# Kernel optimization log

Measured on AMD Instinct MI355X. Metric: run time of the kernel, lower is better.

## Reference

```python
import jax, jax.numpy as jnp
import numpy as np

D_MODEL = 512
H = 8


def setup_inputs() -> dict:
    key = jax.random.key(0)
    ks = jax.random.split(key, 11)
    B, L, D = 8, 1024, D_MODEL
    s = 1.0 / np.sqrt(D)
    return {
        "q": jax.random.normal(ks[0], (B, L, D), jnp.float32),
        "k": jax.random.normal(ks[1], (B, L, D), jnp.float32),
        "v": jax.random.normal(ks[2], (B, L, D), jnp.float32),
        "Wq": jax.random.normal(ks[3], (D, D), jnp.float32) * s,
        "bq": jnp.zeros((D,), jnp.float32),
        "Wk": jax.random.normal(ks[4], (D, D), jnp.float32) * s,
        "bk": jnp.zeros((D,), jnp.float32),
        "Wv": jax.random.normal(ks[5], (D, D), jnp.float32) * s,
        "bv": jnp.zeros((D,), jnp.float32),
        "Wo": jax.random.normal(ks[6], (D, D), jnp.float32) * s,
        "bo": jnp.zeros((D,), jnp.float32),
    }


def _split_heads(x, h):
    B, L, D = x.shape
    return x.reshape(B, L, h, D // h).transpose(0, 2, 1, 3)  # (B,h,L,dk)


def reference(q, k, v, Wq, bq, Wk, bk, Wv, bv, Wo, bo):
    B, L, D = q.shape
    dk = D // H
    qw = q @ Wq + bq
    kw = k @ Wk + bk
    vw = q @ Wv + bv  # faithful to source bug: dense_v applied to q, not v
    qh = _split_heads(qw, H)
    kh = _split_heads(kw, H)
    vh = _split_heads(vw, H)
    scale = jnp.asarray(1.0 / np.sqrt(dk), qh.dtype)
    scores = jnp.einsum("bhqd,bhkd->bhqk", qh, kh) * scale  # (B,h,L,L)
    attn = jax.nn.softmax(scores, axis=-1)
    ctx = jnp.einsum("bhqk,bhkd->bhqd", attn, vh)  # (B,h,L,dk)
    out = ctx.transpose(0, 2, 1, 3).reshape(B, L, D) @ Wo + bo
    return out, attn
```

## Files before the change

### kernel.cpp

```cpp
#include <hip/hip_runtime.h>

typedef unsigned short u16;
typedef __bf16 bf16x8 __attribute__((ext_vector_type(8)));
typedef unsigned short u16x8 __attribute__((ext_vector_type(8)));
typedef unsigned short u16x4 __attribute__((ext_vector_type(4)));
typedef float f32x4 __attribute__((ext_vector_type(4)));

#define MFMA16(a, b, c) __builtin_amdgcn_mfma_f32_16x16x32_bf16(a, b, c, 0, 0, 0)

__device__ __forceinline__ u16 f2bf(float f) {
    union { float f; unsigned u; } v; v.f = f;
    unsigned r = v.u + 0x7fffu + ((v.u >> 16) & 1u);
    return (u16)(r >> 16);
}
__device__ __forceinline__ float bf2f(u16 u) {
    union { unsigned u; float f; } v; v.u = (unsigned)u << 16;
    return v.f;
}

__global__ __launch_bounds__(256) void wtrans(const float* Wq, const float* Wk,
                                              const float* Wv, const float* Wo, u16* WT) {
    __shared__ float t[32][33];
    const int z = blockIdx.z;
    const float* W = (z == 0) ? Wq : (z == 1) ? Wk : (z == 2) ? Wv : Wo;
    u16* out = WT + (size_t)z * 512 * 512;
    const int tx = threadIdx.x, ty = threadIdx.y;
    const int k0 = blockIdx.y * 32, n0 = blockIdx.x * 32;
#pragma unroll
    for (int p = 0; p < 4; ++p)
        t[ty + 8 * p][tx] = W[(size_t)(k0 + ty + 8 * p) * 512 + n0 + tx];
    __syncthreads();
#pragma unroll
    for (int p = 0; p < 4; ++p) {
        const int n = n0 + ty + 8 * p;
        out[(size_t)n * 512 + k0 + tx] = f2bf(t[tx][ty + 8 * p]);
    }
}

__global__ __launch_bounds__(256) void qkconv(const float* q, const float* k, u16* qb, u16* kb) {
    const size_t n4 = (size_t)8192 * 512 / 4;
    const size_t stride = (size_t)gridDim.x * 256;
    for (size_t i = (size_t)blockIdx.x * 256 + threadIdx.x; i < 2 * n4; i += stride) {
        const float4 v = (i < n4) ? ((const float4*)q)[i] : ((const float4*)k)[i - n4];
        u16x4 o;
        o[0] = f2bf(v.x); o[1] = f2bf(v.y); o[2] = f2bf(v.z); o[3] = f2bf(v.w);
        if (i < n4) ((u16x4*)qb)[i] = o; else ((u16x4*)kb)[i - n4] = o;
    }
}

template <bool C_F32>
__device__ __forceinline__ void gemm_core(const u16* A, const u16* Bt,
                                          const float* bias, void* Cp,
                                          int bm, int bn) {
    __shared__ u16 As[128 * 72];
    __shared__ u16 Bs[128 * 72];
    const int tid  = threadIdx.x;
    const int lane = tid & 63;
    const int w    = tid >> 6;
    const int wm   = (w >> 1) * 64;
    const int wn   = (w & 1) * 64;
    const int col  = lane & 15;
    const int quad = lane >> 4;

    f32x4 acc[4][4] = {};

    for (int kt = 0; kt < 512; kt += 64) {
        __syncthreads();
        {
            const int kg = (tid & 7) * 8;
            const int r0 = tid >> 3;
#pragma unroll
            for (int p = 0; p < 4; ++p) {
                const int r = r0 + p * 32;
                *(u16x8*)(As + r * 72 + kg) =
                    *(const u16x8*)(A + (size_t)(bm * 128 + r) * 512 + kt + kg);
                *(u16x8*)(Bs + r * 72 + kg) =
                    *(const u16x8*)(Bt + (size_t)(bn * 128 + r) * 512 + kt + kg);
            }
        }
        __syncthreads();
#pragma unroll
        for (int ks = 0; ks < 2; ++ks) {
            const int k0 = ks * 32 + quad * 8;
            bf16x8 af[4], bfr[4];
#pragma unroll
            for (int i = 0; i < 4; ++i)
                af[i] = __builtin_bit_cast(bf16x8, *(const u16x8*)(As + (wm + i * 16 + col) * 72 + k0));
#pragma unroll
            for (int j = 0; j < 4; ++j)
                bfr[j] = __builtin_bit_cast(bf16x8, *(const u16x8*)(Bs + (wn + j * 16 + col) * 72 + k0));
#pragma unroll
            for (int i = 0; i < 4; ++i)
#pragma unroll
                for (int j = 0; j < 4; ++j)
                    acc[i][j] = MFMA16(af[i], bfr[j], acc[i][j]);
        }
    }
#pragma unroll
    for (int j = 0; j < 4; ++j) {
        const int gn = bn * 128 + wn + j * 16 + col;
        const float bv = bias[gn];
#pragma unroll
        for (int i = 0; i < 4; ++i) {
#pragma unroll
            for (int r = 0; r < 4; ++r) {
                const int gm = bm * 128 + wm + i * 16 + quad * 4 + r;
                const float val = acc[i][j][r] + bv;
                if (C_F32) ((float*)Cp)[(size_t)gm * 512 + gn] = val;
                else       ((u16*)Cp)[(size_t)gm * 512 + gn]   = f2bf(val);
            }
        }
    }
}

__global__ __launch_bounds__(256, 3) void qkv_gemm(const u16* qb, const u16* kb, const u16* WT,
                                                   const float* bq, const float* bk, const float* bv,
                                                   u16* out) {
    const int z = blockIdx.z;
    const u16* A      = (z == 1) ? kb : qb;
    const u16* B      = WT + (size_t)z * 512 * 512;
    const float* bias = (z == 0) ? bq : (z == 1) ? bk : bv;
    u16* C            = out + (size_t)z * 8192 * 512;
    gemm_core<false>(A, B, bias, C, blockIdx.x, blockIdx.y);
}

__global__ __launch_bounds__(256, 3) void out_gemm(const u16* ctx, const u16* WoT,
                                                   const float* bo, float* out) {
    gemm_core<true>(ctx, WoT, bo, out, blockIdx.x, blockIdx.y);
}

__global__ __launch_bounds__(512, 4) void attn_kernel(const u16* qw, const u16* kw, const u16* vw,
                                                      float* attn_out, u16* ctx) {
    __shared__ u16 Ks[64 * 72];
    __shared__ u16 Vt[64 * 72];
    __shared__ u16 Ps[8][16 * 72];

    const int qt  = blockIdx.x;
    const int bh  = blockIdx.y;
    const int b   = bh >> 3, h = bh & 7;
    const int tid = threadIdx.x;
    const int lane = tid & 63, w = tid >> 6;
    const int col = lane & 15, quad = lane >> 4;
    const int wq  = w * 16;
    const float scale = 0.125f;

    const size_t headbase = (size_t)b * 1024 * 512 + (size_t)h * 64;

    bf16x8 qf[2];
    {
        const size_t qrow = headbase + (size_t)(qt * 128 + wq + col) * 512 + quad * 8;
        qf[0] = __builtin_bit_cast(bf16x8, *(const u16x8*)(qw + qrow));
        qf[1] = __builtin_bit_cast(bf16x8, *(const u16x8*)(qw + qrow + 32));
    }

    float l_acc[4] = {0.f, 0.f, 0.f, 0.f};

    for (int kt = 0; kt < 16; ++kt) {
        __syncthreads();
        {
            const int key = tid >> 3, kg = (tid & 7) * 8;
            *(u16x8*)(Ks + key * 72 + kg) =
                *(const u16x8*)(kw + headbase + (size_t)(kt * 64 + key) * 512 + kg);
        }
        __syncthreads();
        f32x4 s[4] = {};
#pragma unroll
        for (int ks = 0; ks < 2; ++ks) {
            const int k0 = ks * 32 + quad * 8;
            bf16x8 kf[4];
#pragma unroll
            for (int j = 0; j < 4; ++j)
                kf[j] = __builtin_bit_cast(bf16x8, *(const u16x8*)(Ks + (j * 16 + col) * 72 + k0));
#pragma unroll
            for (int j = 0; j < 4; ++j)
                s[j] = MFMA16(qf[ks], kf[j], s[j]);
        }
#pragma unroll
        for (int r = 0; r < 4; ++r)
            l_acc[r] += __expf(s[0][r] * scale) + __expf(s[1][r] * scale) +
                        __expf(s[2][r] * scale) + __expf(s[3][r] * scale);
    }

    float rinv[4];
#pragma unroll
    for (int r = 0; r < 4; ++r) {
        float l = l_acc[r];
        l += __shfl_xor(l, 1); l += __shfl_xor(l, 2);
        l += __shfl_xor(l, 4); l += __shfl_xor(l, 8);
        rinv[r] = 1.0f / l;
    }

    f32x4 o[4] = {};

    for (int kt = 0; kt < 16; ++kt) {
        __syncthreads();
        {
            const int key = tid >> 3, kg = (tid & 7) * 8;
            *(u16x8*)(Ks + key * 72 + kg) =
                *(const u16x8*)(kw + headbase + (size_t)(kt * 64 + key) * 512 + kg);
        }
        {
            const int key = tid & 63, oct = tid >> 6;
            const u16x8 vv = *(const u16x8*)(vw + headbase + (size_t)(kt * 64 + key) * 512 + oct * 8);
#pragma unroll
            for (int e = 0; e < 8; ++e)
                Vt[(oct * 8 + e) * 72 + key] = vv[e];
        }
        __syncthreads();
        f32x4 s[4] = {};
#pragma unroll
        for (int ks = 0; ks < 2; ++ks) {
            const int k0 = ks * 32 + quad * 8;
            bf16x8 kf[4];
#pragma unroll
            for (int j = 0; j < 4; ++j)
                kf[j] = __builtin_bit_cast(bf16x8, *(const u16x8*)(Ks + (j * 16 + col) * 72 + k0));
#pragma unroll
            for (int j = 0; j < 4; ++j)
                s[j] = MFMA16(qf[ks], kf[j], s[j]);
        }
#pragma unroll
        for (int j = 0; j < 4; ++j)
#pragma unroll
            for (int r = 0; r < 4; ++r) {
                const float p = __expf(s[j][r] * scale) * rinv[r];
                Ps[w][(quad * 4 + r) * 72 + j * 16 + col] = f2bf(p);
            }
        const int c4 = col * 4;
#pragma unroll
        for (int it = 0; it < 4; ++it) {
            const int rl = it * 4 + quad;
            const u16x4 pv = *(const u16x4*)(&Ps[w][rl * 72 + c4]);
            float4 f;
            f.x = bf2f(pv[0]); f.y = bf2f(pv[1]); f.z = bf2f(pv[2]); f.w = bf2f(pv[3]);
            *(float4*)(attn_out + ((size_t)bh * 1024 + qt * 128 + wq + rl) * 1024
                       + (size_t)kt * 64 + c4) = f;
        }
#pragma unroll
        for (int ks = 0; ks < 2; ++ks) {
            const int k0 = ks * 32 + quad * 8;
            const bf16x8 pf = __builtin_bit_cast(bf16x8, *(const u16x8*)(&Ps[w][col * 72 + k0]));
#pragma unroll
            for (int j = 0; j < 4; ++j) {
                const bf16x8 vf = __builtin_bit_cast(bf16x8, *(const u16x8*)(Vt + (j * 16 + col) * 72 + k0));
                o[j] = MFMA16(pf, vf, o[j]);
            }
        }
    }

#pragma unroll
    for (int j = 0; j < 4; ++j)
#pragma unroll
        for (int r = 0; r < 4; ++r) {
            const int qg = qt * 128 + wq + quad * 4 + r;
            ctx[(size_t)(b * 1024 + qg) * 512 + h * 64 + j * 16 + col] = f2bf(o[j][r]);
        }
}

extern "C" void kernel_launch(void* const* d_in, const int* in_sizes, int n_in,
                              void* d_out, int out_size, void* d_ws, size_t ws_size,
                              hipStream_t stream) {
    (void)in_sizes; (void)n_in; (void)out_size; (void)ws_size;
    const float* q  = (const float*)d_in[0];
    const float* k  = (const float*)d_in[1];
    const float* Wq = (const float*)d_in[3];
    const float* bq = (const float*)d_in[4];
    const float* Wk = (const float*)d_in[5];
    const float* bk = (const float*)d_in[6];
    const float* Wv = (const float*)d_in[7];
    const float* bv = (const float*)d_in[8];
    const float* Wo = (const float*)d_in[9];
    const float* bo = (const float*)d_in[10];

    float* out  = (float*)d_out;
    float* attn = (float*)d_out + (size_t)8 * 1024 * 512;

    char* ws = (char*)d_ws;
    u16* WT  = (u16*)ws;
    u16* qb  = (u16*)(ws + (size_t)2 * 1024 * 1024);
    u16* kb  = qb + (size_t)8192 * 512;
    u16* qkv = kb + (size_t)8192 * 512;
    u16* qw  = qkv;
    u16* kw  = qkv + (size_t)8192 * 512;
    u16* vw  = qkv + (size_t)2 * 8192 * 512;
    u16* ctx = qkv + (size_t)3 * 8192 * 512;

    wtrans     <<<dim3(16, 16, 4), dim3(32, 8), 0, stream>>>(Wq, Wk, Wv, Wo, WT);
    qkconv     <<<dim3(2048),      256,          0, stream>>>(q, k, qb, kb);
    qkv_gemm   <<<dim3(64, 4, 3),  256,          0, stream>>>(qb, kb, WT, bq, bk, bv, qkv);
    attn_kernel<<<dim3(8, 64),     512,          0, stream>>>(qw, kw, vw, attn, ctx);
    out_gemm   <<<dim3(64, 4),     256,          0, stream>>>(ctx, WT + (size_t)3 * 512 * 512, bo, out);
}
```

Before: 444.3 us.

## Pretranspose V, use direct global-to-LDS GEMM loads, enlarge attention key tiles with prefetch

A new vtrans kernel writes V per head in transposed layout, so the attention kernel no longer scatters V into shared memory element by element. The attention kernel now processes 128-key tiles with register prefetch of the next K/V tile, which halves the loop trips and barriers, and writes attn in wider row chunks. The GEMM core switches to global_load_lds 16-byte direct loads into unpadded shared tiles. The costs are one extra launch and an extra pass over V, possible LDS bank conflicts from dropping the GEMM padding, and more shared memory per attention block, which may reduce occupancy.

```diff
diff --git a/kernel.cpp b/kernel.cpp
--- a/kernel.cpp
+++ b/kernel.cpp
@@ -16,6 +16,12 @@
 __device__ __forceinline__ float bf2f(u16 u) {
     union { unsigned u; float f; } v; v.u = (unsigned)u << 16;
     return v.f;
+}
+
+typedef __attribute__((address_space(1))) void GAS;
+typedef __attribute__((address_space(3))) void LAS;
+__device__ __forceinline__ void gload_lds16(const void* g, void* l) {
+    __builtin_amdgcn_global_load_lds((GAS*)g, (LAS*)l, 16, 0, 0);
 }
 
 __global__ __launch_bounds__(256) void wtrans(const float* Wq, const float* Wk,
@@ -48,12 +54,34 @@
     }
 }
 
+__global__ __launch_bounds__(256) void vtrans(const u16* vw, u16* vt) {
+    __shared__ u16 t[64][72];
+    const int l0 = blockIdx.x * 64, h = blockIdx.y, b = blockIdx.z;
+    const int tid = threadIdx.x;
+    {
+        const int r = tid >> 2, c16 = (tid & 3) * 16;
+        const u16* src = vw + (size_t)(b * 1024 + l0 + r) * 512 + h * 64 + c16;
+        *(u16x8*)(&t[r][c16])     = *(const u16x8*)(src);
+        *(u16x8*)(&t[r][c16 + 8]) = *(const u16x8*)(src + 8);
+    }
+    __syncthreads();
+    {
+        const int dk = tid >> 2, lc = (tid & 3) * 16;
+        u16x8 a0, a1;
+#pragma unroll
+        for (int e = 0; e < 8; ++e) { a0[e] = t[lc + e][dk]; a1[e] = t[lc + 8 + e][dk]; }
+        u16* dst = vt + ((size_t)(b * 8 + h) * 64 + dk) * 1024 + l0 + lc;
+        *(u16x8*)dst       = a0;
+        *(u16x8*)(dst + 8) = a1;
+    }
+}
+
 template <bool C_F32>
 __device__ __forceinline__ void gemm_core(const u16* A, const u16* Bt,
                                           const float* bias, void* Cp,
                                           int bm, int bn) {
-    __shared__ u16 As[128 * 72];
-    __shared__ u16 Bs[128 * 72];
+    __shared__ u16 As[128 * 64];
+    __shared__ u16 Bs[128 * 64];
     const int tid  = threadIdx.x;
     const int lane = tid & 63;
     const int w    = tid >> 6;
@@ -61,22 +89,19 @@
     const int wn   = (w & 1) * 64;
     const int col  = lane & 15;
     const int quad = lane >> 4;
+    const int srow = lane >> 3;
+    const int scol = (lane & 7) * 8;
 
     f32x4 acc[4][4] = {};
 
     for (int kt = 0; kt < 512; kt += 64) {
         __syncthreads();
-        {
-            const int kg = (tid & 7) * 8;
-            const int r0 = tid >> 3;
-#pragma unroll
-            for (int p = 0; p < 4; ++p) {
-                const int r = r0 + p * 32;
-                *(u16x8*)(As + r * 72 + kg) =
-                    *(const u16x8*)(A + (size_t)(bm * 128 + r) * 512 + kt + kg);
-                *(u16x8*)(Bs + r * 72 + kg) =
-                    *(const u16x8*)(Bt + (size_t)(bn * 128 + r) * 512 + kt + kg);
-            }
+#pragma unroll
+        for (int p = 0; p < 4; ++p) {
+            const int c  = w * 4 + p;
+            const int gr = c * 8 + srow;
+            gload_lds16(A  + (size_t)(bm * 128 + gr) * 512 + kt + scol, As + c * 512);
+            gload_lds16(Bt + (size_t)(bn * 128 + gr) * 512 + kt + scol, Bs + c * 512);
         }
         __syncthreads();
 #pragma unroll
@@ -85,10 +110,10 @@
             bf16x8 af[4], bfr[4];
 #pragma unroll
             for (int i = 0; i < 4; ++i)
-                af[i] = __builtin_bit_cast(bf16x8, *(const u16x8*)(As + (wm + i * 16 + col) * 72 + k0));
+                af[i] = __builtin_bit_cast(bf16x8, *(const u16x8*)(As + (wm + i * 16 + col) * 64 + k0));
 #pragma unroll
             for (int j = 0; j < 4; ++j)
-                bfr[j] = __builtin_bit_cast(bf16x8, *(const u16x8*)(Bs + (wn + j * 16 + col) * 72 + k0));
+                bfr[j] = __builtin_bit_cast(bf16x8, *(const u16x8*)(Bs + (wn + j * 16 + col) * 64 + k0));
 #pragma unroll
             for (int i = 0; i < 4; ++i)
 #pragma unroll
@@ -129,11 +154,11 @@
     gemm_core<true>(ctx, WoT, bo, out, blockIdx.x, blockIdx.y);
 }
 
-__global__ __launch_bounds__(512, 4) void attn_kernel(const u16* qw, const u16* kw, const u16* vw,
+__global__ __launch_bounds__(512, 4) void attn_kernel(const u16* qw, const u16* kw, const u16* vt,
                                                       float* attn_out, u16* ctx) {
-    __shared__ u16 Ks[64 * 72];
-    __shared__ u16 Vt[64 * 72];
-    __shared__ u16 Ps[8][16 * 72];
+    __shared__ u16 Ks[128 * 72];
+    __shared__ u16 Vs[64 * 136];
+    __shared__ u16 Ps[8][16 * 136];
 
     const int qt  = blockIdx.x;
     const int bh  = blockIdx.y;
@@ -144,41 +169,51 @@
     const int wq  = w * 16;
     const float scale = 0.125f;
 
-    const size_t headbase = (size_t)b * 1024 * 512 + (size_t)h * 64;
+    const size_t headbase = (size_t)b * (1024 * 512) + (size_t)h * 64;
+    const u16* vh = vt + (size_t)bh * (64 * 1024);
+
+    const int krow = tid >> 2, koff = (tid & 3) * 16;
+    const int vrow = tid >> 3, voff = (tid & 7) * 16;
+    const u16* kbase = kw + headbase + (size_t)krow * 512 + koff;
+    const u16* vbase = vh + (size_t)vrow * 1024 + voff;
 
     bf16x8 qf[2];
     {
-        const size_t qrow = headbase + (size_t)(qt * 128 + wq + col) * 512 + quad * 8;
-        qf[0] = __builtin_bit_cast(bf16x8, *(const u16x8*)(qw + qrow));
-        qf[1] = __builtin_bit_cast(bf16x8, *(const u16x8*)(qw + qrow + 32));
+        const u16* qp = qw + headbase + (size_t)(qt * 128 + wq + col) * 512 + quad * 8;
+        qf[0] = __builtin_bit_cast(bf16x8, *(const u16x8*)qp);
+        qf[1] = __builtin_bit_cast(bf16x8, *(const u16x8*)(qp + 32));
     }
 
     float l_acc[4] = {0.f, 0.f, 0.f, 0.f};
 
-    for (int kt = 0; kt < 16; ++kt) {
-        __syncthreads();
-        {
-            const int key = tid >> 3, kg = (tid & 7) * 8;
-            *(u16x8*)(Ks + key * 72 + kg) =
-                *(const u16x8*)(kw + headbase + (size_t)(kt * 64 + key) * 512 + kg);
-        }
-        __syncthreads();
-        f32x4 s[4] = {};
+    u16x8 rk0 = *(const u16x8*)kbase;
+    u16x8 rk1 = *(const u16x8*)(kbase + 8);
+    for (int kt = 0; kt < 8; ++kt) {
+        __syncthreads();
+        *(u16x8*)(Ks + krow * 72 + koff)     = rk0;
+        *(u16x8*)(Ks + krow * 72 + koff + 8) = rk1;
+        __syncthreads();
+        if (kt < 7) {
+            const u16* kp = kbase + (size_t)(kt + 1) * (128 * 512);
+            rk0 = *(const u16x8*)kp;
+            rk1 = *(const u16x8*)(kp + 8);
+        }
+        f32x4 s[8] = {};
 #pragma unroll
         for (int ks = 0; ks < 2; ++ks) {
             const int k0 = ks * 32 + quad * 8;
-            bf16x8 kf[4];
-#pragma unroll
-            for (int j = 0; j < 4; ++j)
-                kf[j] = __builtin_bit_cast(bf16x8, *(const u16x8*)(Ks + (j * 16 + col) * 72 + k0));
-#pragma unroll
-            for (int j = 0; j < 4; ++j)
-                s[j] = MFMA16(qf[ks], kf[j], s[j]);
-        }
-#pragma unroll
-        for (int r = 0; r < 4; ++r)
-            l_acc[r] += __expf(s[0][r] * scale) + __expf(s[1][r] * scale) +
-                        __expf(s[2][r] * scale) + __expf(s[3][r] * scale);
+#pragma unroll
+            for (int j = 0; j < 8; ++j) {
+                const bf16x8 kf = __builtin_bit_cast(bf16x8,
+                    *(const u16x8*)(Ks + (j * 16 + col) * 72 + k0));
+                s[j] = MFMA16(qf[ks], kf, s[j]);
+            }
+        }
+#pragma unroll
+        for (int j = 0; j < 8; ++j)
+#pragma unroll
+            for (int r = 0; r < 4; ++r)
+                l_acc[r] += __expf(s[j][r] * scale);
     }
 
     float rinv[4];
@@ -192,57 +227,67 @@
 
     f32x4 o[4] = {};
 
-    for (int kt = 0; kt < 16; ++kt) {
-        __syncthreads();
+    rk0 = *(const u16x8*)kbase;
+    rk1 = *(const u16x8*)(kbase + 8);
+    u16x8 rv0 = *(const u16x8*)vbase;
+    u16x8 rv1 = *(const u16x8*)(vbase + 8);
+    for (int kt = 0; kt < 8; ++kt) {
+        __syncthreads();
+        *(u16x8*)(Ks + krow * 72 + koff)      = rk0;
+        *(u16x8*)(Ks + krow * 72 + koff + 8)  = rk1;
+        *(u16x8*)(Vs + vrow * 136 + voff)     = rv0;
+        *(u16x8*)(Vs + vrow * 136 + voff + 8) = rv1;
+        __syncthreads();
+        if (kt < 7) {
+            const u16* kp = kbase + (size_t)(kt + 1) * (128 * 512);
+            rk0 = *(const u16x8*)kp;
+            rk1 = *(const u16x8*)(kp + 8);
+            const u16* vp = vbase + (kt + 1) * 128;
+            rv0 = *(const u16x8*)vp;
+            rv1 = *(const u16x8*)(vp + 8);
+        }
+        u16* pw = &Ps[w][0];
+#pragma unroll
+        for (int half = 0; half < 2; ++half) {
+            f32x4 s[4] = {};
+#pragma unroll
+            for (int ks = 0; ks < 2; ++ks) {
+                const int k0 = ks * 32 + quad * 8;
+#pragma unroll
+                for (int j = 0; j < 4; ++j) {
+                    const bf16x8 kf = __builtin_bit_cast(bf16x8,
+                        *(const u16x8*)(Ks + (half * 64 + j * 16 + col) * 72 + k0));
+                    s[j] = MFMA16(qf[ks], kf, s[j]);
+                }
+            }
+#pragma unroll
+            for (int j = 0; j < 4; ++j)
+#pragma unroll
+                for (int r = 0; r < 4; ++r) {
+                    const float p = __expf(s[j][r] * scale) * rinv[r];
+                    pw[(quad * 4 + r) * 136 + half * 64 + j * 16 + col] = f2bf(p);
+                }
+        }
         {
-            const int key = tid >> 3, kg = (tid & 7) * 8;
-            *(u16x8*)(Ks + key * 72 + kg) =
-                *(const u16x8*)(kw + headbase + (size_t)(kt * 64 + key) * 512 + kg);
-        }
-        {
-            const int key = tid & 63, oct = tid >> 6;
-            const u16x8 vv = *(const u16x8*)(vw + headbase + (size_t)(kt * 64 + key) * 512 + oct * 8);
-#pragma unroll
-            for (int e = 0; e < 8; ++e)
-                Vt[(oct * 8 + e) * 72 + key] = vv[e];
-        }
-        __syncthreads();
-        f32x4 s[4] = {};
-#pragma unroll
-        for (int ks = 0; ks < 2; ++ks) {
+            const int rl = lane >> 2, c0 = (lane & 3) * 4;
+            float* ao = attn_out + ((size_t)bh * 1024 + (size_t)(qt * 128 + wq + rl)) * 1024
+                        + (size_t)kt * 128 + c0;
+#pragma unroll
+            for (int it = 0; it < 8; ++it) {
+                const u16x4 pv = *(const u16x4*)(pw + rl * 136 + it * 16 + c0);
+                float4 f;
+                f.x = bf2f(pv[0]); f.y = bf2f(pv[1]); f.z = bf2f(pv[2]); f.w = bf2f(pv[3]);
+                *(float4*)(ao + it * 16) = f;
+            }
+        }
+#pragma unroll
+        for (int ks = 0; ks < 4; ++ks) {
             const int k0 = ks * 32 + quad * 8;
-            bf16x8 kf[4];
-#pragma unroll
-            for (int j = 0; j < 4; ++j)
-                kf[j] = __builtin_bit_cast(bf16x8, *(const u16x8*)(Ks + (j * 16 + col) * 72 + k0));
-#pragma unroll
-            for (int j = 0; j < 4; ++j)
-                s[j] = MFMA16(qf[ks], kf[j], s[j]);
-        }
-#pragma unroll
-        for (int j = 0; j < 4; ++j)
-#pragma unroll
-            for (int r = 0; r < 4; ++r) {
-                const float p = __expf(s[j][r] * scale) * rinv[r];
-                Ps[w][(quad * 4 + r) * 72 + j * 16 + col] = f2bf(p);
-            }
-        const int c4 = col * 4;
-#pragma unroll
-        for (int it = 0; it < 4; ++it) {
-            const int rl = it * 4 + quad;
-            const u16x4 pv = *(const u16x4*)(&Ps[w][rl * 72 + c4]);
-            float4 f;
-            f.x = bf2f(pv[0]); f.y = bf2f(pv[1]); f.z = bf2f(pv[2]); f.w = bf2f(pv[3]);
-            *(float4*)(attn_out + ((size_t)bh * 1024 + qt * 128 + wq + rl) * 1024
-                       + (size_t)kt * 64 + c4) = f;
-        }
-#pragma unroll
-        for (int ks = 0; ks < 2; ++ks) {
-            const int k0 = ks * 32 + quad * 8;
-            const bf16x8 pf = __builtin_bit_cast(bf16x8, *(const u16x8*)(&Ps[w][col * 72 + k0]));
+            const bf16x8 pf = __builtin_bit_cast(bf16x8, *(const u16x8*)(pw + col * 136 + k0));
 #pragma unroll
             for (int j = 0; j < 4; ++j) {
-                const bf16x8 vf = __builtin_bit_cast(bf16x8, *(const u16x8*)(Vt + (j * 16 + col) * 72 + k0));
+                const bf16x8 vf = __builtin_bit_cast(bf16x8,
+                    *(const u16x8*)(Vs + (j * 16 + col) * 136 + k0));
                 o[j] = MFMA16(pf, vf, o[j]);
             }
         }
@@ -284,10 +329,12 @@
     u16* kw  = qkv + (size_t)8192 * 512;
     u16* vw  = qkv + (size_t)2 * 8192 * 512;
     u16* ctx = qkv + (size_t)3 * 8192 * 512;
+    u16* vt  = qkv + (size_t)4 * 8192 * 512;
 
     wtrans     <<<dim3(16, 16, 4), dim3(32, 8), 0, stream>>>(Wq, Wk, Wv, Wo, WT);
     qkconv     <<<dim3(2048),      256,          0, stream>>>(q, k, qb, kb);
     qkv_gemm   <<<dim3(64, 4, 3),  256,          0, stream>>>(qb, kb, WT, bq, bk, bv, qkv);
-    attn_kernel<<<dim3(8, 64),     512,          0, stream>>>(qw, kw, vw, attn, ctx);
+    vtrans     <<<dim3(16, 8, 8),  256,          0, stream>>>(vw, vt);
+    attn_kernel<<<dim3(8, 64),     512,          0, stream>>>(qw, kw, vt, attn, ctx);
     out_gemm   <<<dim3(64, 4),     256,          0, stream>>>(ctx, WT + (size_t)3 * 512 * 512, bo, out);
 }
```

Result: faster. 415.7 us (-6.4%).
